# Optimization experiments

Hardware: AMD Instinct MI355X
Metric: run time of the kernel (lower is better)

The kernel has to match this reference:

```python
import jax, jax.numpy as jnp
import numpy as np

NUM_TAGS = 32            # init arg
N = NUM_TAGS + 2         # internal num_tags (start/end appended)
START = N - 2
END = N - 1
B = 1024
T = 1024
NEG = -6969.0            # module's 'minus infinity' constant


def setup_inputs() -> dict:
    key = jax.random.key(0)
    k1, k2 = jax.random.split(key)
    features = jax.random.normal(k1, (B, T, N), dtype=jnp.float32)
    # learned parameter: transition matrix [N, N]
    transitions = jax.random.normal(k2, (N, N), dtype=jnp.float32)
    return {"features": features, "transitions": transitions}


def _viterbi(features, transitions):
    # features: [B, T, N]; transitions: [N, N]
    Bn, Tn, Nn = features.shape
    init = jnp.full((Bn, Nn), NEG, dtype=features.dtype).at[:, START].set(0.0)

    def step(scores, feat):
        # score[b, j, k] = scores[b, k] + feat[b, j] + transitions[j, k]
        sc = scores[:, None, :] + feat[:, :, None] + transitions[None, :, :]
        return jnp.max(sc, axis=-1), jnp.argmax(sc, axis=-1)

    feats_t = jnp.swapaxes(features, 0, 1)            # [T, B, N]
    scores, paths = jax.lax.scan(step, init, feats_t)  # paths: [T, B, N] int

    scores = scores + transitions[END]                # add transition to end tag
    best = jnp.max(scores, axis=-1)                   # [B]
    idx = jnp.argmax(scores, axis=-1)                 # [B]

    # backtrack through backpointers, from t = T-1 down to 0
    def back(i, path):
        ni = jnp.take_along_axis(path, i[:, None], axis=1)[:, 0]
        return ni, ni

    _, tags = jax.lax.scan(back, idx, paths, reverse=True)  # tags: [T, B]
    best_path = jnp.concatenate([tags.T, idx[:, None]], axis=1)  # [B, T+1]
    return best, best_path


def reference(features, transitions):
    return _viterbi(features, transitions)
```

## Files before the change

### kernel.cpp

```cpp
#include <hip/hip_runtime.h>
#include <stdint.h>

#define BB 1024
#define TT 1024
#define NN 34
#define NEGV -6969.0f

typedef float v2f __attribute__((ext_vector_type(2)));

__device__ __forceinline__ v2f pk_add(v2f a, v2f b) {
    v2f d;
    asm("v_pk_add_f32 %0, %1, %2" : "=v"(d) : "v"(a), "v"(b));
    return d;
}

__device__ __forceinline__ float rdlane_f(float v, int l) {
    return __int_as_float(__builtin_amdgcn_readlane(__float_as_int(v), l));
}

__global__ __launch_bounds__(64, 1) void viterbi_wave(
        const float* __restrict__ feat,
        const float* __restrict__ trans,
        float* __restrict__ out)
{
    __shared__ unsigned char bp[TT * NN];
    __shared__ __align__(16) float sc[64];
    __shared__ unsigned char Fm[16 * NN];

    const int lane = threadIdx.x;
    const int bg   = blockIdx.x;
    const int jc   = (lane < NN) ? lane : (NN - 1);

    v2f tr2[17];
#pragma unroll
    for (int p = 0; p < 17; ++p) {
        tr2[p].x = trans[jc * NN + 2 * p];
        tr2[p].y = trans[jc * NN + 2 * p + 1];
    }
    const float trE = trans[33 * NN + jc];

    const float* fp = feat + (size_t)bg * TT * NN + jc;
    float fr0 = fp[0 * NN], fr1 = fp[1 * NN], fr2 = fp[2 * NN], fr3 = fp[3 * NN];

    v2f sk2[17];
#pragma unroll
    for (int p = 0; p < 17; ++p) { sk2[p].x = NEGV; sk2[p].y = NEGV; }
    sk2[16].x = 0.0f;

    float m = NEGV;
    int tbase = 0;

    auto vstep = [&](float f) {
        v2f f2; f2.x = f; f2.y = f;
        v2f q[17];
#pragma unroll
        for (int p = 0; p < 17; ++p) q[p] = pk_add(pk_add(sk2[p], f2), tr2[p]);

        float pm[17];
#pragma unroll
        for (int p = 0; p < 17; ++p) pm[p] = fmaxf(q[p].x, q[p].y);
        float u0 = fmaxf(fmaxf(pm[0], pm[1]),   fmaxf(pm[2], pm[3]));
        float u1 = fmaxf(fmaxf(pm[4], pm[5]),   fmaxf(pm[6], pm[7]));
        float u2 = fmaxf(fmaxf(pm[8], pm[9]),   fmaxf(pm[10], pm[11]));
        float u3 = fmaxf(fmaxf(pm[12], pm[13]), fmaxf(pm[14], pm[15]));
        float mx = fmaxf(fmaxf(fmaxf(u0, u1), fmaxf(u2, u3)), pm[16]);

        sc[lane] = mx;
#pragma unroll
        for (int p = 0; p < 17; ++p) sk2[p] = *(const v2f*)&sc[2 * p];

        int am0 = 127, am1 = 127, am2 = 127, am3 = 127;
#pragma unroll
        for (int p = 16; p >= 0; --p) {
            int k0 = 2 * p, k1 = 2 * p + 1;
            bool e1 = (q[p].y == mx);
            if ((k1 & 3) == 0) am0 = e1 ? k1 : am0;
            else if ((k1 & 3) == 1) am1 = e1 ? k1 : am1;
            else if ((k1 & 3) == 2) am2 = e1 ? k1 : am2;
            else am3 = e1 ? k1 : am3;
            bool e0 = (q[p].x == mx);
            if ((k0 & 3) == 0) am0 = e0 ? k0 : am0;
            else if ((k0 & 3) == 1) am1 = e0 ? k0 : am1;
            else if ((k0 & 3) == 2) am2 = e0 ? k0 : am2;
            else am3 = e0 ? k0 : am3;
        }
        int am = min(min(am0, am1), min(am2, am3));

        if (lane < NN) bp[tbase + lane] = (unsigned char)am;
        tbase += NN;
        m = mx;
    };

    for (int n = 0; n < 255; ++n) {
        { float f = fr0; fr0 = fp[4 * NN]; vstep(f); }
        { float f = fr1; fr1 = fp[5 * NN]; vstep(f); }
        { float f = fr2; fr2 = fp[6 * NN]; vstep(f); }
        { float f = fr3; fr3 = fp[7 * NN]; vstep(f); }
        fp += 4 * NN;
    }
    vstep(fr0); vstep(fr1); vstep(fr2); vstep(fr3);

    float fs = m + trE;
    float bm = rdlane_f(fs, 0);
    int bi = 0;
#pragma unroll
    for (int k = 1; k < NN; ++k) {
        float v = rdlane_f(fs, k);
        bool g = (v > bm);
        bm = g ? v : bm;
        bi = g ? k : bi;
    }
    if (lane == 0) out[bg] = bm;

    int cc[9], xx[9], mm[9], cb[9];
#pragma unroll
    for (int r = 0; r < 9; ++r) {
        int job = 64 * r + lane;
        if (job > 543) job = 543;
        cc[r] = job / 34;
        xx[r] = job - 34 * cc[r];
        mm[r] = xx[r];
        cb[r] = cc[r] * (64 * NN);
    }
    for (int i = 63; i >= 0; --i) {
        int ib = i * NN;
#pragma unroll
        for (int r = 0; r < 9; ++r) mm[r] = bp[cb[r] + ib + mm[r]];
    }
#pragma unroll
    for (int r = 0; r < 9; ++r) Fm[cc[r] * NN + xx[r]] = (unsigned char)mm[r];

    int e = bi;
    int myeb = (lane == 15) ? e : 0;
#pragma unroll
    for (int c2 = 15; c2 >= 1; --c2) {
        e = Fm[c2 * NN + e];
        myeb = (lane == c2 - 1) ? e : myeb;
    }

    float* po = out + BB + (size_t)bg * (TT + 1);
    if (lane < 16) {
        int mm2 = myeb;
        int base = lane * (64 * NN);
        for (int i = 63; i >= 0; --i) {
            mm2 = bp[base + i * NN + mm2];
            po[lane * 64 + i] = (float)mm2;
        }
    }
    if (lane == 16) po[TT] = (float)bi;
}

extern "C" void kernel_launch(void* const* d_in, const int* in_sizes, int n_in,
                              void* d_out, int out_size, void* d_ws, size_t ws_size,
                              hipStream_t stream) {
    const float* feat  = (const float*)d_in[0];
    const float* trans = (const float*)d_in[1];
    float* out = (float*)d_out;

    viterbi_wave<<<BB, 64, 0, stream>>>(feat, trans, out);
}
```

Before: 604.8 us.

## Pack four backpointer steps per LDS word and read scores with 128-bit loads

```diff
diff --git a/kernel.cpp b/kernel.cpp
--- a/kernel.cpp
+++ b/kernel.cpp
@@ -7,15 +7,18 @@
 #define NEGV -6969.0f
 
 typedef float v2f __attribute__((ext_vector_type(2)));
+typedef float v4f __attribute__((ext_vector_type(4)));
 
 __device__ __forceinline__ v2f pk_add(v2f a, v2f b) {
     v2f d;
     asm("v_pk_add_f32 %0, %1, %2" : "=v"(d) : "v"(a), "v"(b));
     return d;
 }
-
 __device__ __forceinline__ float rdlane_f(float v, int l) {
     return __int_as_float(__builtin_amdgcn_readlane(__float_as_int(v), l));
+}
+__device__ __forceinline__ float M3(float a, float b, float c) {
+    return fmaxf(fmaxf(a, b), c);
 }
 
 __global__ __launch_bounds__(64, 1) void viterbi_wave(
@@ -23,7 +26,7 @@
         const float* __restrict__ trans,
         float* __restrict__ out)
 {
-    __shared__ unsigned char bp[TT * NN];
+    __shared__ unsigned int bp32[256 * NN];
     __shared__ __align__(16) float sc[64];
     __shared__ unsigned char Fm[16 * NN];
 
@@ -39,66 +42,80 @@
     }
     const float trE = trans[33 * NN + jc];
 
-    const float* fp = feat + (size_t)bg * TT * NN + jc;
-    float fr0 = fp[0 * NN], fr1 = fp[1 * NN], fr2 = fp[2 * NN], fr3 = fp[3 * NN];
+    const float* fpp = feat + (size_t)bg * TT * NN + jc;
+    float fr0 = fpp[0 * NN], fr1 = fpp[1 * NN], fr2 = fpp[2 * NN], fr3 = fpp[3 * NN];
 
-    v2f sk2[17];
+    v4f skv[9];
 #pragma unroll
-    for (int p = 0; p < 17; ++p) { sk2[p].x = NEGV; sk2[p].y = NEGV; }
-    sk2[16].x = 0.0f;
+    for (int r = 0; r < 9; ++r) { skv[r].x = NEGV; skv[r].y = NEGV; skv[r].z = NEGV; skv[r].w = NEGV; }
+    skv[8].x = 0.0f;
 
     float m = NEGV;
-    int tbase = 0;
 
-    auto vstep = [&](float f) {
+    auto vstep = [&](float f) -> int {
         v2f f2; f2.x = f; f2.y = f;
-        v2f q[17];
+        v2f q2[17];
 #pragma unroll
-        for (int p = 0; p < 17; ++p) q[p] = pk_add(pk_add(sk2[p], f2), tr2[p]);
-
-        float pm[17];
-#pragma unroll
-        for (int p = 0; p < 17; ++p) pm[p] = fmaxf(q[p].x, q[p].y);
-        float u0 = fmaxf(fmaxf(pm[0], pm[1]),   fmaxf(pm[2], pm[3]));
-        float u1 = fmaxf(fmaxf(pm[4], pm[5]),   fmaxf(pm[6], pm[7]));
-        float u2 = fmaxf(fmaxf(pm[8], pm[9]),   fmaxf(pm[10], pm[11]));
-        float u3 = fmaxf(fmaxf(pm[12], pm[13]), fmaxf(pm[14], pm[15]));
-        float mx = fmaxf(fmaxf(fmaxf(u0, u1), fmaxf(u2, u3)), pm[16]);
+        for (int p = 0; p < 17; ++p) {
+            v2f sp = (p & 1)
+                ? __builtin_shufflevector(skv[p >> 1], skv[p >> 1], 2, 3)
+                : __builtin_shufflevector(skv[p >> 1], skv[p >> 1], 0, 1);
+            q2[p] = pk_add(pk_add(sp, f2), tr2[p]);
+        }
+        float t0  = M3(q2[0].x,  q2[0].y,  q2[1].x);
+        float t1  = M3(q2[1].y,  q2[2].x,  q2[2].y);
+        float t2  = M3(q2[3].x,  q2[3].y,  q2[4].x);
+        float t3  = M3(q2[4].y,  q2[5].x,  q2[5].y);
+        float t4  = M3(q2[6].x,  q2[6].y,  q2[7].x);
+        float t5  = M3(q2[7].y,  q2[8].x,  q2[8].y);
+        float t6  = M3(q2[9].x,  q2[9].y,  q2[10].x);
+        float t7  = M3(q2[10].y, q2[11].x, q2[11].y);
+        float t8  = M3(q2[12].x, q2[12].y, q2[13].x);
+        float t9  = M3(q2[13].y, q2[14].x, q2[14].y);
+        float t10 = M3(q2[15].x, q2[15].y, q2[16].x);
+        float u0 = M3(t0, t1, t2);
+        float u1 = M3(t3, t4, t5);
+        float u2 = M3(t6, t7, t8);
+        float u3 = M3(t9, t10, q2[16].y);
+        float mx = fmaxf(fmaxf(u0, u1), fmaxf(u2, u3));
 
         sc[lane] = mx;
 #pragma unroll
-        for (int p = 0; p < 17; ++p) sk2[p] = *(const v2f*)&sc[2 * p];
+        for (int r = 0; r < 9; ++r) skv[r] = *(const v4f*)(&sc[4 * r]);
 
-        int am0 = 127, am1 = 127, am2 = 127, am3 = 127;
+        int am0 = 255, am1 = 255, am2 = 255, am3 = 255;
 #pragma unroll
-        for (int p = 16; p >= 0; --p) {
-            int k0 = 2 * p, k1 = 2 * p + 1;
-            bool e1 = (q[p].y == mx);
-            if ((k1 & 3) == 0) am0 = e1 ? k1 : am0;
-            else if ((k1 & 3) == 1) am1 = e1 ? k1 : am1;
-            else if ((k1 & 3) == 2) am2 = e1 ? k1 : am2;
-            else am3 = e1 ? k1 : am3;
-            bool e0 = (q[p].x == mx);
-            if ((k0 & 3) == 0) am0 = e0 ? k0 : am0;
-            else if ((k0 & 3) == 1) am1 = e0 ? k0 : am1;
-            else if ((k0 & 3) == 2) am2 = e0 ? k0 : am2;
-            else am3 = e0 ? k0 : am3;
+        for (int k = 33; k >= 0; --k) {
+            float vk = (k & 1) ? q2[k >> 1].y : q2[k >> 1].x;
+            bool e = (vk == mx);
+            if ((k & 3) == 0) am0 = e ? k : am0;
+            else if ((k & 3) == 1) am1 = e ? k : am1;
+            else if ((k & 3) == 2) am2 = e ? k : am2;
+            else am3 = e ? k : am3;
         }
-        int am = min(min(am0, am1), min(am2, am3));
-
-        if (lane < NN) bp[tbase + lane] = (unsigned char)am;
-        tbase += NN;
         m = mx;
+        return min(min(am0, am1), min(am2, am3));
     };
 
+    int wofs = lane;
     for (int n = 0; n < 255; ++n) {
-        { float f = fr0; fr0 = fp[4 * NN]; vstep(f); }
-        { float f = fr1; fr1 = fp[5 * NN]; vstep(f); }
-        { float f = fr2; fr2 = fp[6 * NN]; vstep(f); }
-        { float f = fr3; fr3 = fp[7 * NN]; vstep(f); }
-        fp += 4 * NN;
+        int a0, a1, a2, a3;
+        { float f = fr0; fr0 = fpp[4 * NN]; a0 = vstep(f); }
+        { float f = fr1; fr1 = fpp[5 * NN]; a1 = vstep(f); }
+        { float f = fr2; fr2 = fpp[6 * NN]; a2 = vstep(f); }
+        { float f = fr3; fr3 = fpp[7 * NN]; a3 = vstep(f); }
+        unsigned u = (unsigned)a0 | ((unsigned)a1 << 8) |
+                     ((unsigned)a2 << 16) | ((unsigned)a3 << 24);
+        if (lane < NN) bp32[wofs] = u;
+        wofs += NN;
+        fpp += 4 * NN;
     }
-    vstep(fr0); vstep(fr1); vstep(fr2); vstep(fr3);
+    {
+        int a0 = vstep(fr0), a1 = vstep(fr1), a2 = vstep(fr2), a3 = vstep(fr3);
+        unsigned u = (unsigned)a0 | ((unsigned)a1 << 8) |
+                     ((unsigned)a2 << 16) | ((unsigned)a3 << 24);
+        if (lane < NN) bp32[wofs] = u;
+    }
 
     float fs = m + trE;
     float bm = rdlane_f(fs, 0);
@@ -112,6 +129,8 @@
     }
     if (lane == 0) out[bg] = bm;
 
+    const unsigned char* bpb = (const unsigned char*)bp32;
+
     int cc[9], xx[9], mm[9], cb[9];
 #pragma unroll
     for (int r = 0; r < 9; ++r) {
@@ -120,12 +139,12 @@
         cc[r] = job / 34;
         xx[r] = job - 34 * cc[r];
         mm[r] = xx[r];
-        cb[r] = cc[r] * (64 * NN);
+        cb[r] = cc[r] * 2176;
     }
     for (int i = 63; i >= 0; --i) {
-        int ib = i * NN;
+        int ioff = ((i >> 2) * 136) + (i & 3);
 #pragma unroll
-        for (int r = 0; r < 9; ++r) mm[r] = bp[cb[r] + ib + mm[r]];
+        for (int r = 0; r < 9; ++r) mm[r] = bpb[cb[r] + ioff + 4 * mm[r]];
     }
 #pragma unroll
     for (int r = 0; r < 9; ++r) Fm[cc[r] * NN + xx[r]] = (unsigned char)mm[r];
@@ -141,9 +160,9 @@
     float* po = out + BB + (size_t)bg * (TT + 1);
     if (lane < 16) {
         int mm2 = myeb;
-        int base = lane * (64 * NN);
+        int base = lane * 2176;
         for (int i = 63; i >= 0; --i) {
-            mm2 = bp[base + i * NN + mm2];
+            mm2 = bpb[base + ((i >> 2) * 136) + (i & 3) + 4 * mm2];
             po[lane * 64 + i] = (float)mm2;
         }
     }
@@ -156,6 +175,7 @@
     const float* feat  = (const float*)d_in[0];
     const float* trans = (const float*)d_in[1];
     float* out = (float*)d_out;
+    (void)d_ws; (void)ws_size;
 
     viterbi_wave<<<BB, 64, 0, stream>>>(feat, trans, out);
 }
```

Result: no change. 609.2 us (+0.7%).
